# Optimization experiments

Measured on AMD Instinct MI355X. Metric: run time of the kernel, lower is better.

The kernel has to match this reference:

```python
import jax, jax.numpy as jnp
import numpy as np

B = 8192
D = 256
TEMP = 0.05
EPS = 1e-5
NORM_EPS = 1e-12  # F.normalize default eps


def _l2norm(x):
    n = jnp.linalg.norm(x, axis=1, keepdims=True)
    return x / jnp.maximum(n, NORM_EPS)


def setup_inputs() -> dict:
    key = jax.random.key(0)
    kq, kk = jax.random.split(key)
    q = jax.random.normal(kq, (B, D), dtype=jnp.float32)
    k = jax.random.normal(kk, (B, D), dtype=jnp.float32)
    return {"q": q, "k": k}


def reference(q, k):
    qn = _l2norm(q)
    kn = _l2norm(k)
    # Only the off-diagonal BxB blocks of the (2B,2B) similarity matrix are
    # used: sim[:B, B:] = qn @ kn.T and sim[B:, :B] = its transpose.
    S = jnp.einsum('id,jd->ij', qn, kn)            # [B, B] cosine sims
    E = jnp.exp(S / TEMP)                          # exp(sim / T)
    d = jnp.diagonal(E)                            # nominator_qk == nominator_kq
    off_sum_rows = E.sum(axis=1) - d               # masked row sums (qk negatives)
    off_sum_cols = E.sum(axis=0) - d               # masked col sums (kq negatives)
    den_qk = d + off_sum_rows
    den_kq = d + off_sum_cols
    loss_qk = jnp.sum(-jnp.log(d / den_qk + EPS)) / B
    loss_kq = jnp.sum(-jnp.log(d / den_kq + EPS)) / B
    return loss_qk + loss_kq
```

## Files before the change

### kernel.cpp

```cpp
#include <hip/hip_runtime.h>
#include <hip/hip_bf16.h>


#define NB 8192
#define ND 256

constexpr float EPS = 1e-5f;
constexpr float EXP2_SCALE = 28.853900817779268f;

typedef float f32x4 __attribute__((ext_vector_type(4)));
typedef int   i32x8 __attribute__((ext_vector_type(8)));


__global__ __launch_bounds__(1024) void norm_pack_kernel(
    const float* __restrict__ q, const float* __restrict__ k,
    uint* __restrict__ qp, uint* __restrict__ kp, float* __restrict__ diag,
    float* __restrict__ out) {
  __shared__ uint lq[16 * 68];
  __shared__ uint lk[16 * 68];
  if (blockIdx.x == 0 && threadIdx.x == 0) out[0] = 0.f;

  const int w    = threadIdx.x >> 6;
  const int lane = threadIdx.x & 63;
  const int row  = blockIdx.x * 16 + w;
  const float4* q4 = reinterpret_cast<const float4*>(q + (size_t)row * ND);
  const float4* k4 = reinterpret_cast<const float4*>(k + (size_t)row * ND);
  float4 qv = q4[lane];
  float4 kv = k4[lane];
  float sq = qv.x * qv.x + qv.y * qv.y + qv.z * qv.z + qv.w * qv.w;
  float sk = kv.x * kv.x + kv.y * kv.y + kv.z * kv.z + kv.w * kv.w;
  float dp = qv.x * kv.x + qv.y * kv.y + qv.z * kv.z + qv.w * kv.w;
#pragma unroll
  for (int m = 1; m < 64; m <<= 1) {
    sq += __shfl_xor(sq, m);
    sk += __shfl_xor(sk, m);
    dp += __shfl_xor(dp, m);
  }
  const float iq = 1.0f / fmaxf(sqrtf(sq), 1e-12f);
  const float ik = 1.0f / fmaxf(sqrtf(sk), 1e-12f);
  int dq = __builtin_amdgcn_cvt_pk_fp8_f32(qv.x * iq, qv.y * iq, 0, false);
  dq = __builtin_amdgcn_cvt_pk_fp8_f32(qv.z * iq, qv.w * iq, dq, true);
  int dk = __builtin_amdgcn_cvt_pk_fp8_f32(kv.x * ik, kv.y * ik, 0, false);
  dk = __builtin_amdgcn_cvt_pk_fp8_f32(kv.z * ik, kv.w * ik, dk, true);
  lq[w * 68 + lane] = (uint)dq;
  lk[w * 68 + lane] = (uint)dk;
  if (lane == 0) diag[row] = __expf(dp * iq * ik * 20.0f);
  __syncthreads();

  const int t = threadIdx.x;
  if (t < 512) {
    const int tt = t & 255;
    const int u  = tt >> 1;
    const int h  = tt & 1;
    const int ul = u & 63;
    const int ks = u >> 6;
    const int src_dw = (ul & 15) * 68 + ks * 32 + (ul >> 4) * 8 + h * 4;
    const uint* Ls = (t < 256) ? lq : lk;
    uint4 v = *reinterpret_cast<const uint4*>(&Ls[src_dw]);
    uint* dst = (t < 256) ? qp : kp;
    reinterpret_cast<uint4*>(dst)[(size_t)blockIdx.x * 256 + tt] = v;
  }
}

#define BT 128

__global__ __launch_bounds__(256, 4) void gemm_exp_reduce_kernel(
    const uint* __restrict__ qp, const uint* __restrict__ kp,
    float* __restrict__ RowP, float* __restrict__ ColP) {
  __shared__ float RS[128 * 3];
  __shared__ float CS[128 * 3];

  const int tid  = threadIdx.x;
  const int lane = tid & 63;
  const int wave = tid >> 6;
  const int wr = wave >> 1;
  const int wc = wave & 1;
  const int l15 = lane & 15;
  const int lhi = lane >> 4;

  const int lid = blockIdx.y * 64 + blockIdx.x;
  const int xcd = lid & 7;
  const int j   = lid >> 3;
  const int rb  = (xcd >> 2) * 32 + (j >> 4);
  const int cb  = (xcd & 3) * 16 + (j & 15);
  const int brow = rb * BT;
  const int bcol = cb * BT;

  const i32x8* qp8 = reinterpret_cast<const i32x8*>(qp);
  const i32x8* kp8 = reinterpret_cast<const i32x8*>(kp);
  const int qg0 = (brow >> 4) + wr * 4;
  const int kg0 = (bcol >> 4) + wc * 4;

  f32x4 acc[4][4];
#pragma unroll
  for (int kg = 0; kg < 4; ++kg)
#pragma unroll
    for (int qg = 0; qg < 4; ++qg)
      acc[kg][qg] = (f32x4){0.f, 0.f, 0.f, 0.f};

#pragma unroll
  for (int ks = 0; ks < 2; ++ks) {
    i32x8 kf[4];
#pragma unroll
    for (int kg = 0; kg < 4; ++kg)
      kf[kg] = kp8[(size_t)(kg0 + kg) * 128 + ks * 64 + lane];
#pragma unroll
    for (int qg = 0; qg < 4; ++qg) {
      const i32x8 qf = qp8[(size_t)(qg0 + qg) * 128 + ks * 64 + lane];
#pragma unroll
      for (int kg = 0; kg < 4; ++kg)
        acc[kg][qg] = __builtin_amdgcn_mfma_scale_f32_16x16x128_f8f6f4(
            kf[kg], qf, acc[kg][qg], 0, 0, 0, 0x7F7F7F7F, 0, 0x7F7F7F7F);
    }
  }

#pragma unroll
  for (int kg = 0; kg < 4; ++kg)
#pragma unroll
    for (int qg = 0; qg < 4; ++qg)
#pragma unroll
      for (int j2 = 0; j2 < 4; ++j2)
        acc[kg][qg][j2] = exp2f(acc[kg][qg][j2] * EXP2_SCALE);

  float rs[4];
#pragma unroll
  for (int qg = 0; qg < 4; ++qg) {
    f32x4 s4 = (acc[0][qg] + acc[1][qg]) + (acc[2][qg] + acc[3][qg]);
    float v = (s4[0] + s4[1]) + (s4[2] + s4[3]);
    v += __shfl_xor(v, 16);
    v += __shfl_xor(v, 32);
    rs[qg] = v;
  }
  {
    float val = (lhi == 0) ? rs[0] : (lhi == 1) ? rs[1] : (lhi == 2) ? rs[2] : rs[3];
    RS[(wr * 64 + lhi * 16 + l15) * 3 + wc] = val;
  }

  float c[4][4];
#pragma unroll
  for (int kg = 0; kg < 4; ++kg)
#pragma unroll
    for (int j2 = 0; j2 < 4; ++j2)
      c[kg][j2] = (acc[kg][0][j2] + acc[kg][1][j2]) +
                  (acc[kg][2][j2] + acc[kg][3][j2]);
  const bool b0 = (l15 & 1), b1 = (l15 & 2), b2 = (l15 & 4), b3 = (l15 & 8);
  float d[4][2];
#pragma unroll
  for (int kg = 0; kg < 4; ++kg) {
#pragma unroll
    for (int jh = 0; jh < 2; ++jh) {
      float t = b0 ? c[kg][jh * 2] : c[kg][jh * 2 + 1];
      float u = __shfl_xor(t, 1);
      d[kg][jh] = (b0 ? c[kg][jh * 2 + 1] : c[kg][jh * 2]) + u;
    }
  }
  float e[4];
#pragma unroll
  for (int kg = 0; kg < 4; ++kg) {
    float t = b1 ? d[kg][0] : d[kg][1];
    float u = __shfl_xor(t, 2);
    e[kg] = (b1 ? d[kg][1] : d[kg][0]) + u;
  }
  float g01, g23;
  {
    float t, u;
    t = b2 ? e[0] : e[1]; u = __shfl_xor(t, 4); g01 = (b2 ? e[1] : e[0]) + u;
    t = b2 ? e[2] : e[3]; u = __shfl_xor(t, 4); g23 = (b2 ? e[3] : e[2]) + u;
  }
  float f;
  {
    float t = b3 ? g01 : g23;
    float u = __shfl_xor(t, 8);
    f = (b3 ? g23 : g01) + u;
  }
  CS[(wc * 64 + (l15 >> 2) * 16 + lhi * 4 + (l15 & 3)) * 3 + wr] = f;
  __syncthreads();

  if (tid < 128) {
    RowP[(size_t)cb * NB + brow + tid] = RS[tid * 3 + 0] + RS[tid * 3 + 1];
  } else {
    const int t = tid - 128;
    ColP[(size_t)rb * NB + bcol + t] = CS[t * 3 + 0] + CS[t * 3 + 1];
  }
}

__global__ __launch_bounds__(256) void loss_kernel(
    const float* __restrict__ diag, const float* __restrict__ RowP,
    const float* __restrict__ ColP, float* __restrict__ out) {
  const int i = blockIdx.x * 256 + threadIdx.x;
  float rs = 0.f, cs = 0.f;
#pragma unroll 8
  for (int j = 0; j < 64; ++j) {
    rs += RowP[(size_t)j * NB + i];
    cs += ColP[(size_t)j * NB + i];
  }
  const float d = diag[i];
  float acc = -__logf(d / rs + EPS) - __logf(d / cs + EPS);
#pragma unroll
  for (int m = 1; m < 64; m <<= 1) acc += __shfl_xor(acc, m);
  __shared__ float ls[4];
  const int wave = threadIdx.x >> 6;
  if ((threadIdx.x & 63) == 0) ls[wave] = acc;
  __syncthreads();
  if (threadIdx.x == 0)
    atomicAdd(out, (ls[0] + ls[1] + ls[2] + ls[3]) * (1.0f / NB));
}

extern "C" void kernel_launch(void* const* d_in, const int* in_sizes, int n_in,
                              void* d_out, int out_size, void* d_ws, size_t ws_size,
                              hipStream_t stream) {
  const float* q = (const float*)d_in[0];
  const float* k = (const float*)d_in[1];
  char* ws = (char*)d_ws;
  uint*  qp   = (uint*)ws;
  uint*  kp   = (uint*)(ws + (size_t)NB * ND);
  float* diag = (float*)(ws + (size_t)2 * NB * ND);
  float* RowP = diag + NB;
  float* ColP = RowP + 64 * NB;
  float* out  = (float*)d_out;

  norm_pack_kernel<<<NB / 16, 1024, 0, stream>>>(q, k, qp, kp, diag, out);
  gemm_exp_reduce_kernel<<<dim3(64, 64), 256, 0, stream>>>(qp, kp, RowP, ColP);
  loss_kernel<<<32, 256, 0, stream>>>(diag, RowP, ColP, out);
}
```

Measured before the change: 48.67 us.

## Stage fp8 GEMM tiles into LDS via global_load_lds with XOR swizzle

```diff
diff --git a/kernel.cpp b/kernel.cpp
--- a/kernel.cpp
+++ b/kernel.cpp
@@ -9,7 +9,13 @@
 constexpr float EXP2_SCALE = 28.853900817779268f;
 
 typedef float f32x4 __attribute__((ext_vector_type(4)));
+typedef int   i32x4 __attribute__((ext_vector_type(4)));
 typedef int   i32x8 __attribute__((ext_vector_type(8)));
+
+#define GLOAD_LDS16(g, l)                                                  \
+  __builtin_amdgcn_global_load_lds(                                        \
+      (const __attribute__((address_space(1))) unsigned int*)(g),          \
+      (__attribute__((address_space(3))) unsigned int*)(l), 16, 0, 0)
 
 
 __global__ __launch_bounds__(1024) void norm_pack_kernel(
@@ -65,8 +71,10 @@
 #define BT 128
 
 __global__ __launch_bounds__(256, 4) void gemm_exp_reduce_kernel(
-    const uint* __restrict__ qp, const uint* __restrict__ kp,
+    const char* __restrict__ qpc, const char* __restrict__ kpc,
     float* __restrict__ RowP, float* __restrict__ ColP) {
+  __shared__ char As[32768];
+  __shared__ char Bs[32768];
   __shared__ float RS[128 * 3];
   __shared__ float CS[128 * 3];
 
@@ -86,10 +94,20 @@
   const int brow = rb * BT;
   const int bcol = cb * BT;
 
-  const i32x8* qp8 = reinterpret_cast<const i32x8*>(qp);
-  const i32x8* kp8 = reinterpret_cast<const i32x8*>(kp);
-  const int qg0 = (brow >> 4) + wr * 4;
-  const int kg0 = (bcol >> 4) + wc * 4;
+  {
+    const int sx = ((tid >> 3) & 1) << 4;
+    const size_t ab = (size_t)rb * 32768;
+    const size_t bb = (size_t)cb * 32768;
+#pragma unroll
+    for (int i = 0; i < 8; ++i) {
+      const int fb = (i * 256 + tid) * 16;
+      GLOAD_LDS16(qpc + ab + (fb ^ sx), As + fb);
+      GLOAD_LDS16(kpc + bb + (fb ^ sx), Bs + fb);
+    }
+  }
+  __syncthreads();
+
+  const int rx = ((lane >> 2) & 1) << 4;
 
   f32x4 acc[4][4];
 #pragma unroll
@@ -98,15 +116,26 @@
     for (int qg = 0; qg < 4; ++qg)
       acc[kg][qg] = (f32x4){0.f, 0.f, 0.f, 0.f};
 
+  auto ldlds = [&](const char* base, int off) -> i32x8 {
+    const int a0 = (off + lane * 32) ^ rx;
+    const int a1 = (off + lane * 32 + 16) ^ rx;
+    i32x4 lo = *reinterpret_cast<const i32x4*>(base + a0);
+    i32x4 hi = *reinterpret_cast<const i32x4*>(base + a1);
+    i32x8 v;
+    v[0] = lo[0]; v[1] = lo[1]; v[2] = lo[2]; v[3] = lo[3];
+    v[4] = hi[0]; v[5] = hi[1]; v[6] = hi[2]; v[7] = hi[3];
+    return v;
+  };
+
 #pragma unroll
   for (int ks = 0; ks < 2; ++ks) {
     i32x8 kf[4];
 #pragma unroll
     for (int kg = 0; kg < 4; ++kg)
-      kf[kg] = kp8[(size_t)(kg0 + kg) * 128 + ks * 64 + lane];
+      kf[kg] = ldlds(Bs, (wc * 4 + kg) * 4096 + ks * 2048);
 #pragma unroll
     for (int qg = 0; qg < 4; ++qg) {
-      const i32x8 qf = qp8[(size_t)(qg0 + qg) * 128 + ks * 64 + lane];
+      const i32x8 qf = ldlds(As, (wr * 4 + qg) * 4096 + ks * 2048);
 #pragma unroll
       for (int kg = 0; kg < 4; ++kg)
         acc[kg][qg] = __builtin_amdgcn_mfma_scale_f32_16x16x128_f8f6f4(
@@ -220,6 +249,7 @@
   float* out  = (float*)d_out;
 
   norm_pack_kernel<<<NB / 16, 1024, 0, stream>>>(q, k, qp, kp, diag, out);
-  gemm_exp_reduce_kernel<<<dim3(64, 64), 256, 0, stream>>>(qp, kp, RowP, ColP);
+  gemm_exp_reduce_kernel<<<dim3(64, 64), 256, 0, stream>>>(
+      (const char*)qp, (const char*)kp, RowP, ColP);
   loss_kernel<<<32, 256, 0, stream>>>(diag, RowP, ColP, out);
 }
```

Result: slower. 57.43 us (+18.0%).

## Persist q fragments in registers and sweep eight column tiles per block

Applied to the files above, without the earlier changes.

```diff
diff --git a/kernel.cpp b/kernel.cpp
--- a/kernel.cpp
+++ b/kernel.cpp
@@ -62,14 +62,9 @@
   }
 }
 
-#define BT 128
-
-__global__ __launch_bounds__(256, 4) void gemm_exp_reduce_kernel(
+__global__ __launch_bounds__(256, 2) void gemm_exp_reduce_kernel(
     const uint* __restrict__ qp, const uint* __restrict__ kp,
     float* __restrict__ RowP, float* __restrict__ ColP) {
-  __shared__ float RS[128 * 3];
-  __shared__ float CS[128 * 3];
-
   const int tid  = threadIdx.x;
   const int lane = tid & 63;
   const int wave = tid >> 6;
@@ -78,110 +73,117 @@
   const int l15 = lane & 15;
   const int lhi = lane >> 4;
 
-  const int lid = blockIdx.y * 64 + blockIdx.x;
+  const int lid = blockIdx.x;
   const int xcd = lid & 7;
   const int j   = lid >> 3;
-  const int rb  = (xcd >> 2) * 32 + (j >> 4);
-  const int cb  = (xcd & 3) * 16 + (j & 15);
-  const int brow = rb * BT;
-  const int bcol = cb * BT;
+  const int rb  = xcd * 8 + (j >> 3);
+  const int cc  = j & 7;
+  const int brow = rb * 128;
+  const int bcol = cc * 1024;
 
   const i32x8* qp8 = reinterpret_cast<const i32x8*>(qp);
   const i32x8* kp8 = reinterpret_cast<const i32x8*>(kp);
   const int qg0 = (brow >> 4) + wr * 4;
-  const int kg0 = (bcol >> 4) + wc * 4;
-
-  f32x4 acc[4][4];
-#pragma unroll
-  for (int kg = 0; kg < 4; ++kg)
-#pragma unroll
-    for (int qg = 0; qg < 4; ++qg)
-      acc[kg][qg] = (f32x4){0.f, 0.f, 0.f, 0.f};
-
-#pragma unroll
-  for (int ks = 0; ks < 2; ++ks) {
-    i32x8 kf[4];
+
+  i32x8 qf[4][2];
+#pragma unroll
+  for (int qg = 0; qg < 4; ++qg)
+#pragma unroll
+    for (int ks = 0; ks < 2; ++ks)
+      qf[qg][ks] = qp8[(size_t)(qg0 + qg) * 128 + ks * 64 + lane];
+
+  float racc[4] = {0.f, 0.f, 0.f, 0.f};
+
+  const bool b0 = (l15 & 1), b1 = (l15 & 2), b2 = (l15 & 4), b3 = (l15 & 8);
+
+  for (int tc = 0; tc < 8; ++tc) {
+    const int kg0 = ((bcol + tc * 128) >> 4) + wc * 4;
+    f32x4 acc[4][4];
 #pragma unroll
     for (int kg = 0; kg < 4; ++kg)
-      kf[kg] = kp8[(size_t)(kg0 + kg) * 128 + ks * 64 + lane];
+#pragma unroll
+      for (int qg = 0; qg < 4; ++qg)
+        acc[kg][qg] = (f32x4){0.f, 0.f, 0.f, 0.f};
+
+#pragma unroll
+    for (int ks = 0; ks < 2; ++ks) {
+      i32x8 kf[4];
+#pragma unroll
+      for (int kg = 0; kg < 4; ++kg)
+        kf[kg] = kp8[(size_t)(kg0 + kg) * 128 + ks * 64 + lane];
+#pragma unroll
+      for (int qg = 0; qg < 4; ++qg)
+#pragma unroll
+        for (int kg = 0; kg < 4; ++kg)
+          acc[kg][qg] = __builtin_amdgcn_mfma_scale_f32_16x16x128_f8f6f4(
+              kf[kg], qf[qg][ks], acc[kg][qg], 0, 0, 0,
+              0x7F7F7F7F, 0, 0x7F7F7F7F);
+    }
+
+#pragma unroll
+    for (int kg = 0; kg < 4; ++kg)
+#pragma unroll
+      for (int qg = 0; qg < 4; ++qg)
+#pragma unroll
+        for (int j2 = 0; j2 < 4; ++j2)
+          acc[kg][qg][j2] = exp2f(acc[kg][qg][j2] * EXP2_SCALE);
+
 #pragma unroll
     for (int qg = 0; qg < 4; ++qg) {
-      const i32x8 qf = qp8[(size_t)(qg0 + qg) * 128 + ks * 64 + lane];
-#pragma unroll
-      for (int kg = 0; kg < 4; ++kg)
-        acc[kg][qg] = __builtin_amdgcn_mfma_scale_f32_16x16x128_f8f6f4(
-            kf[kg], qf, acc[kg][qg], 0, 0, 0, 0x7F7F7F7F, 0, 0x7F7F7F7F);
-    }
-  }
-
-#pragma unroll
-  for (int kg = 0; kg < 4; ++kg)
-#pragma unroll
-    for (int qg = 0; qg < 4; ++qg)
+      f32x4 s4 = (acc[0][qg] + acc[1][qg]) + (acc[2][qg] + acc[3][qg]);
+      racc[qg] += (s4[0] + s4[1]) + (s4[2] + s4[3]);
+    }
+
+    float c[4][4];
+#pragma unroll
+    for (int kg = 0; kg < 4; ++kg)
 #pragma unroll
       for (int j2 = 0; j2 < 4; ++j2)
-        acc[kg][qg][j2] = exp2f(acc[kg][qg][j2] * EXP2_SCALE);
-
-  float rs[4];
-#pragma unroll
-  for (int qg = 0; qg < 4; ++qg) {
-    f32x4 s4 = (acc[0][qg] + acc[1][qg]) + (acc[2][qg] + acc[3][qg]);
-    float v = (s4[0] + s4[1]) + (s4[2] + s4[3]);
-    v += __shfl_xor(v, 16);
-    v += __shfl_xor(v, 32);
-    rs[qg] = v;
-  }
+        c[kg][j2] = (acc[kg][0][j2] + acc[kg][1][j2]) +
+                    (acc[kg][2][j2] + acc[kg][3][j2]);
+    float d[4][2];
+#pragma unroll
+    for (int kg = 0; kg < 4; ++kg) {
+#pragma unroll
+      for (int jh = 0; jh < 2; ++jh) {
+        float t = b0 ? c[kg][jh * 2] : c[kg][jh * 2 + 1];
+        float u = __shfl_xor(t, 1);
+        d[kg][jh] = (b0 ? c[kg][jh * 2 + 1] : c[kg][jh * 2]) + u;
+      }
+    }
+    float e[4];
+#pragma unroll
+    for (int kg = 0; kg < 4; ++kg) {
+      float t = b1 ? d[kg][0] : d[kg][1];
+      float u = __shfl_xor(t, 2);
+      e[kg] = (b1 ? d[kg][1] : d[kg][0]) + u;
+    }
+    float g01, g23;
+    {
+      float t, u;
+      t = b2 ? e[0] : e[1]; u = __shfl_xor(t, 4); g01 = (b2 ? e[1] : e[0]) + u;
+      t = b2 ? e[2] : e[3]; u = __shfl_xor(t, 4); g23 = (b2 ? e[3] : e[2]) + u;
+    }
+    float f;
+    {
+      float t = b3 ? g01 : g23;
+      float u = __shfl_xor(t, 8);
+      f = (b3 ? g23 : g01) + u;
+    }
+    ColP[(size_t)(rb * 2 + wr) * NB + bcol + tc * 128 + wc * 64 +
+         (l15 >> 2) * 16 + lhi * 4 + (l15 & 3)] = f;
+  }
+
+  float v0, v1, v2, v3;
   {
-    float val = (lhi == 0) ? rs[0] : (lhi == 1) ? rs[1] : (lhi == 2) ? rs[2] : rs[3];
-    RS[(wr * 64 + lhi * 16 + l15) * 3 + wc] = val;
-  }
-
-  float c[4][4];
-#pragma unroll
-  for (int kg = 0; kg < 4; ++kg)
-#pragma unroll
-    for (int j2 = 0; j2 < 4; ++j2)
-      c[kg][j2] = (acc[kg][0][j2] + acc[kg][1][j2]) +
-                  (acc[kg][2][j2] + acc[kg][3][j2]);
-  const bool b0 = (l15 & 1), b1 = (l15 & 2), b2 = (l15 & 4), b3 = (l15 & 8);
-  float d[4][2];
-#pragma unroll
-  for (int kg = 0; kg < 4; ++kg) {
-#pragma unroll
-    for (int jh = 0; jh < 2; ++jh) {
-      float t = b0 ? c[kg][jh * 2] : c[kg][jh * 2 + 1];
-      float u = __shfl_xor(t, 1);
-      d[kg][jh] = (b0 ? c[kg][jh * 2 + 1] : c[kg][jh * 2]) + u;
-    }
-  }
-  float e[4];
-#pragma unroll
-  for (int kg = 0; kg < 4; ++kg) {
-    float t = b1 ? d[kg][0] : d[kg][1];
-    float u = __shfl_xor(t, 2);
-    e[kg] = (b1 ? d[kg][1] : d[kg][0]) + u;
-  }
-  float g01, g23;
-  {
-    float t, u;
-    t = b2 ? e[0] : e[1]; u = __shfl_xor(t, 4); g01 = (b2 ? e[1] : e[0]) + u;
-    t = b2 ? e[2] : e[3]; u = __shfl_xor(t, 4); g23 = (b2 ? e[3] : e[2]) + u;
-  }
-  float f;
-  {
-    float t = b3 ? g01 : g23;
-    float u = __shfl_xor(t, 8);
-    f = (b3 ? g23 : g01) + u;
-  }
-  CS[(wc * 64 + (l15 >> 2) * 16 + lhi * 4 + (l15 & 3)) * 3 + wr] = f;
-  __syncthreads();
-
-  if (tid < 128) {
-    RowP[(size_t)cb * NB + brow + tid] = RS[tid * 3 + 0] + RS[tid * 3 + 1];
-  } else {
-    const int t = tid - 128;
-    ColP[(size_t)rb * NB + bcol + t] = CS[t * 3 + 0] + CS[t * 3 + 1];
-  }
+    float t;
+    t = racc[0]; t += __shfl_xor(t, 16); t += __shfl_xor(t, 32); v0 = t;
+    t = racc[1]; t += __shfl_xor(t, 16); t += __shfl_xor(t, 32); v1 = t;
+    t = racc[2]; t += __shfl_xor(t, 16); t += __shfl_xor(t, 32); v2 = t;
+    t = racc[3]; t += __shfl_xor(t, 16); t += __shfl_xor(t, 32); v3 = t;
+  }
+  const float val = (lhi == 0) ? v0 : (lhi == 1) ? v1 : (lhi == 2) ? v2 : v3;
+  RowP[(size_t)(cc * 2 + wc) * NB + brow + wr * 64 + lhi * 16 + l15] = val;
 }
 
 __global__ __launch_bounds__(256) void loss_kernel(
@@ -189,11 +191,10 @@
     const float* __restrict__ ColP, float* __restrict__ out) {
   const int i = blockIdx.x * 256 + threadIdx.x;
   float rs = 0.f, cs = 0.f;
+#pragma unroll 4
+  for (int j = 0; j < 16; ++j) rs += RowP[(size_t)j * NB + i];
 #pragma unroll 8
-  for (int j = 0; j < 64; ++j) {
-    rs += RowP[(size_t)j * NB + i];
-    cs += ColP[(size_t)j * NB + i];
-  }
+  for (int j = 0; j < 128; ++j) cs += ColP[(size_t)j * NB + i];
   const float d = diag[i];
   float acc = -__logf(d / rs + EPS) - __logf(d / cs + EPS);
 #pragma unroll
@@ -216,10 +217,10 @@
   uint*  kp   = (uint*)(ws + (size_t)NB * ND);
   float* diag = (float*)(ws + (size_t)2 * NB * ND);
   float* RowP = diag + NB;
-  float* ColP = RowP + 64 * NB;
+  float* ColP = RowP + 16 * NB;
   float* out  = (float*)d_out;
 
   norm_pack_kernel<<<NB / 16, 1024, 0, stream>>>(q, k, qp, kp, diag, out);
-  gemm_exp_reduce_kernel<<<dim3(64, 64), 256, 0, stream>>>(qp, kp, RowP, ColP);
+  gemm_exp_reduce_kernel<<<512, 256, 0, stream>>>(qp, kp, RowP, ColP);
   loss_kernel<<<32, 256, 0, stream>>>(diag, RowP, ColP, out);
 }
```

New measurement: 48.88 us. Within noise of the previous version (+0.4%).

## Make GEMM blocks persistent over q tiles, keeping k fragments in registers

Applied to the files above, without the earlier changes.

```diff
diff --git a/kernel.cpp b/kernel.cpp
--- a/kernel.cpp
+++ b/kernel.cpp
@@ -10,6 +10,12 @@
 
 typedef float f32x4 __attribute__((ext_vector_type(4)));
 typedef int   i32x8 __attribute__((ext_vector_type(8)));
+
+__device__ __forceinline__ float fast_exp2(float x) {
+  float r;
+  asm("v_exp_f32 %0, %1" : "=v"(r) : "v"(x));
+  return r;
+}
 
 
 __global__ __launch_bounds__(1024) void norm_pack_kernel(
@@ -62,88 +68,92 @@
   }
 }
 
-#define BT 128
-
-__global__ __launch_bounds__(256, 4) void gemm_exp_reduce_kernel(
+__global__ __launch_bounds__(256, 2) void gemm_exp_reduce_kernel(
     const uint* __restrict__ qp, const uint* __restrict__ kp,
     float* __restrict__ RowP, float* __restrict__ ColP) {
-  __shared__ float RS[128 * 3];
-  __shared__ float CS[128 * 3];
-
   const int tid  = threadIdx.x;
   const int lane = tid & 63;
   const int wave = tid >> 6;
-  const int wr = wave >> 1;
-  const int wc = wave & 1;
+  const int wq = wave >> 1;
+  const int wk = wave & 1;
   const int l15 = lane & 15;
   const int lhi = lane >> 4;
 
-  const int lid = blockIdx.y * 64 + blockIdx.x;
-  const int xcd = lid & 7;
-  const int j   = lid >> 3;
-  const int rb  = (xcd >> 2) * 32 + (j >> 4);
-  const int cb  = (xcd & 3) * 16 + (j & 15);
-  const int brow = rb * BT;
-  const int bcol = cb * BT;
+  const int lid = blockIdx.x;
+  const int qc  = lid & 7;
+  const int kb  = lid >> 3;
 
   const i32x8* qp8 = reinterpret_cast<const i32x8*>(qp);
   const i32x8* kp8 = reinterpret_cast<const i32x8*>(kp);
-  const int qg0 = (brow >> 4) + wr * 4;
-  const int kg0 = (bcol >> 4) + wc * 4;
-
-  f32x4 acc[4][4];
+
+  const int kg0 = kb * 8 + wk * 4;
+  i32x8 kf[4][2];
 #pragma unroll
   for (int kg = 0; kg < 4; ++kg)
 #pragma unroll
-    for (int qg = 0; qg < 4; ++qg)
-      acc[kg][qg] = (f32x4){0.f, 0.f, 0.f, 0.f};
-
-#pragma unroll
-  for (int ks = 0; ks < 2; ++ks) {
-    i32x8 kf[4];
+    for (int ks = 0; ks < 2; ++ks)
+      kf[kg][ks] = kp8[(size_t)(kg0 + kg) * 128 + ks * 64 + lane];
+
+  f32x4 cacc[4] = {};
+
+  const bool b0 = (l15 & 1), b1 = (l15 & 2), b2 = (l15 & 4), b3 = (l15 & 8);
+
+  for (int t = 0; t < 8; ++t) {
+    const int qg0 = qc * 64 + t * 8 + wq * 4;
+    f32x4 acc[4][4];
 #pragma unroll
     for (int kg = 0; kg < 4; ++kg)
-      kf[kg] = kp8[(size_t)(kg0 + kg) * 128 + ks * 64 + lane];
+#pragma unroll
+      for (int qg = 0; qg < 4; ++qg)
+        acc[kg][qg] = (f32x4){0.f, 0.f, 0.f, 0.f};
+
+#pragma unroll
+    for (int ks = 0; ks < 2; ++ks) {
+#pragma unroll
+      for (int qg = 0; qg < 4; ++qg) {
+        const i32x8 qf = qp8[(size_t)(qg0 + qg) * 128 + ks * 64 + lane];
+#pragma unroll
+        for (int kg = 0; kg < 4; ++kg)
+          acc[kg][qg] = __builtin_amdgcn_mfma_scale_f32_16x16x128_f8f6f4(
+              kf[kg][ks], qf, acc[kg][qg], 0, 0, 0, 0x7F7F7F7F, 0, 0x7F7F7F7F);
+      }
+    }
+
+#pragma unroll
+    for (int kg = 0; kg < 4; ++kg)
+#pragma unroll
+      for (int qg = 0; qg < 4; ++qg)
+#pragma unroll
+        for (int j2 = 0; j2 < 4; ++j2)
+          acc[kg][qg][j2] = fast_exp2(acc[kg][qg][j2] * EXP2_SCALE);
+
+    float rs[4];
 #pragma unroll
     for (int qg = 0; qg < 4; ++qg) {
-      const i32x8 qf = qp8[(size_t)(qg0 + qg) * 128 + ks * 64 + lane];
-#pragma unroll
-      for (int kg = 0; kg < 4; ++kg)
-        acc[kg][qg] = __builtin_amdgcn_mfma_scale_f32_16x16x128_f8f6f4(
-            kf[kg], qf, acc[kg][qg], 0, 0, 0, 0x7F7F7F7F, 0, 0x7F7F7F7F);
-    }
-  }
-
+      f32x4 s4 = (acc[0][qg] + acc[1][qg]) + (acc[2][qg] + acc[3][qg]);
+      float v = (s4[0] + s4[1]) + (s4[2] + s4[3]);
+      v += __shfl_xor(v, 16);
+      v += __shfl_xor(v, 32);
+      rs[qg] = v;
+    }
+    {
+      const float val = (lhi == 0) ? rs[0] : (lhi == 1) ? rs[1]
+                        : (lhi == 2) ? rs[2] : rs[3];
+      RowP[(size_t)(kb * 2 + wk) * NB + qc * 1024 + t * 128 + wq * 64 +
+           lhi * 16 + l15] = val;
+    }
+
+#pragma unroll
+    for (int kg = 0; kg < 4; ++kg)
+      cacc[kg] += (acc[kg][0] + acc[kg][1]) + (acc[kg][2] + acc[kg][3]);
+  }
+
+  float c[4][4];
 #pragma unroll
   for (int kg = 0; kg < 4; ++kg)
 #pragma unroll
-    for (int qg = 0; qg < 4; ++qg)
-#pragma unroll
-      for (int j2 = 0; j2 < 4; ++j2)
-        acc[kg][qg][j2] = exp2f(acc[kg][qg][j2] * EXP2_SCALE);
-
-  float rs[4];
-#pragma unroll
-  for (int qg = 0; qg < 4; ++qg) {
-    f32x4 s4 = (acc[0][qg] + acc[1][qg]) + (acc[2][qg] + acc[3][qg]);
-    float v = (s4[0] + s4[1]) + (s4[2] + s4[3]);
-    v += __shfl_xor(v, 16);
-    v += __shfl_xor(v, 32);
-    rs[qg] = v;
-  }
-  {
-    float val = (lhi == 0) ? rs[0] : (lhi == 1) ? rs[1] : (lhi == 2) ? rs[2] : rs[3];
-    RS[(wr * 64 + lhi * 16 + l15) * 3 + wc] = val;
-  }
-
-  float c[4][4];
-#pragma unroll
-  for (int kg = 0; kg < 4; ++kg)
-#pragma unroll
     for (int j2 = 0; j2 < 4; ++j2)
-      c[kg][j2] = (acc[kg][0][j2] + acc[kg][1][j2]) +
-                  (acc[kg][2][j2] + acc[kg][3][j2]);
-  const bool b0 = (l15 & 1), b1 = (l15 & 2), b2 = (l15 & 4), b3 = (l15 & 8);
+      c[kg][j2] = cacc[kg][j2];
   float d[4][2];
 #pragma unroll
   for (int kg = 0; kg < 4; ++kg) {
@@ -173,15 +183,8 @@
     float u = __shfl_xor(t, 8);
     f = (b3 ? g23 : g01) + u;
   }
-  CS[(wc * 64 + (l15 >> 2) * 16 + lhi * 4 + (l15 & 3)) * 3 + wr] = f;
-  __syncthreads();
-
-  if (tid < 128) {
-    RowP[(size_t)cb * NB + brow + tid] = RS[tid * 3 + 0] + RS[tid * 3 + 1];
-  } else {
-    const int t = tid - 128;
-    ColP[(size_t)rb * NB + bcol + t] = CS[t * 3 + 0] + CS[t * 3 + 1];
-  }
+  ColP[(size_t)(qc * 2 + wq) * NB + kb * 128 + wk * 64 +
+       (l15 >> 2) * 16 + lhi * 4 + (l15 & 3)] = f;
 }
 
 __global__ __launch_bounds__(256) void loss_kernel(
@@ -190,10 +193,9 @@
   const int i = blockIdx.x * 256 + threadIdx.x;
   float rs = 0.f, cs = 0.f;
 #pragma unroll 8
-  for (int j = 0; j < 64; ++j) {
-    rs += RowP[(size_t)j * NB + i];
-    cs += ColP[(size_t)j * NB + i];
-  }
+  for (int j = 0; j < 128; ++j) rs += RowP[(size_t)j * NB + i];
+#pragma unroll 4
+  for (int j = 0; j < 16; ++j) cs += ColP[(size_t)j * NB + i];
   const float d = diag[i];
   float acc = -__logf(d / rs + EPS) - __logf(d / cs + EPS);
 #pragma unroll
@@ -216,10 +218,10 @@
   uint*  kp   = (uint*)(ws + (size_t)NB * ND);
   float* diag = (float*)(ws + (size_t)2 * NB * ND);
   float* RowP = diag + NB;
-  float* ColP = RowP + 64 * NB;
+  float* ColP = RowP + 128 * NB;
   float* out  = (float*)d_out;
 
   norm_pack_kernel<<<NB / 16, 1024, 0, stream>>>(q, k, qp, kp, diag, out);
-  gemm_exp_reduce_kernel<<<dim3(64, 64), 256, 0, stream>>>(qp, kp, RowP, ColP);
+  gemm_exp_reduce_kernel<<<512, 256, 0, stream>>>(qp, kp, RowP, ColP);
   loss_kernel<<<32, 256, 0, stream>>>(diag, RowP, ColP, out);
 }
```

Result: faster. 43.57 us (-10.5%).
